# Kernel tuning notes

Hardware: AMD Instinct MI355X
Metric: run time of the kernel (lower is better)

The kernel has to match this reference:

```python
import jax, jax.numpy as jnp
import numpy as np

B, L, D, H = 2, 2048, 1024, 16
HD = D // H
ROPE_BASE = 10000.0


def _chain_info(lengths):
    """lengths: [B, L] int, chain lengths packed at the front, zeros after.
    Returns per-position within-chain positions (RoPE resets per chain),
    chain ids, and a validity mask."""
    def one(row):
        csum = jnp.cumsum(row)                      # [L]
        total = csum[-1]
        p = jnp.arange(L)
        cid = jnp.searchsorted(csum, p, side='right')  # chain id per position
        prev = jnp.where(cid > 0, csum[jnp.clip(cid - 1, 0, L - 1)], 0)
        valid = p < total
        pos = jnp.where(valid, p - prev, 0).astype(jnp.float32)
        return pos, cid, valid
    return jax.vmap(one)(lengths)


def _rope_tables(pos):
    # pos: [B, L] float -> cos/sin [B, L, 1, HD]
    inv_freq = 1.0 / (ROPE_BASE ** (jnp.arange(0, HD, 2, dtype=jnp.float32) / HD))
    freqs = pos[..., None] * inv_freq               # [B, L, HD/2]
    emb = jnp.concatenate([freqs, freqs], axis=-1)  # [B, L, HD]
    return jnp.cos(emb)[:, :, None, :], jnp.sin(emb)[:, :, None, :]


def _apply_rope(x, cos, sin):
    d = x.shape[-1]
    x1, x2 = x[..., : d // 2], x[..., d // 2:]
    return x * cos + jnp.concatenate([-x2, x1], axis=-1) * sin


def _branch(x, Wqkv, bqkv, cos, sin, allowed):
    # x: [B, L, D]; allowed: [B, L, L] bool attention mask for this branch
    qkv = x @ Wqkv.T + bqkv                          # [B, L, 3D]
    qkv = qkv.reshape(B, L, 3, H, HD)
    q, k, v = qkv[:, :, 0], qkv[:, :, 1], qkv[:, :, 2]
    q = q * (HD ** -0.5)
    q = _apply_rope(q, cos, sin)
    k = _apply_rope(k, cos, sin)
    scores = jnp.einsum('bthd,bshd->bhts', q, k)     # [B, H, L, L]
    scores = jnp.where(allowed[:, None], scores, -jnp.inf)
    probs = jax.nn.softmax(scores, axis=-1)
    probs = jnp.where(jnp.isnan(probs), 0.0, probs)  # fully-masked rows -> 0
    out = jnp.einsum('bhts,bshd->bthd', probs, v)    # [B, L, H, HD]
    return out.reshape(B, L, D)


def setup_inputs() -> dict:
    key = jax.random.key(0)
    ks = jax.random.split(key, 7)
    s = 0.02
    lens = np.zeros((B, L), np.int64)
    lens[0, :8] = [300, 250, 200, 400, 350, 248, 150, 100]   # sum 1998
    lens[1, :6] = [512, 400, 300, 360, 276, 200]             # sum 2048
    return {
        'hidden_states': jax.random.normal(ks[0], (B, L, D), jnp.float32),
        'attention_mask_in_length': jnp.asarray(lens),
        'Wqkv_intra': jax.random.normal(ks[1], (3 * D, D), jnp.float32) * s,
        'bqkv_intra': jnp.zeros((3 * D,), jnp.float32),
        'Wqkv_inter': jax.random.normal(ks[2], (3 * D, D), jnp.float32) * s,
        'bqkv_inter': jnp.zeros((3 * D,), jnp.float32),
        'Wout': jax.random.normal(ks[3], (D, D), jnp.float32) * s,
        'bout': jnp.zeros((D,), jnp.float32),
    }


def reference(hidden_states, attention_mask_in_length, Wqkv_intra, bqkv_intra,
              Wqkv_inter, bqkv_inter, Wout, bout):
    pos, cid, valid = _chain_info(attention_mask_in_length)
    cos, sin = _rope_tables(pos)
    same_chain = cid[:, :, None] == cid[:, None, :]          # [B, L, L]
    key_valid = valid[:, None, :]                            # [B, 1, L]
    allowed_intra = same_chain & key_valid
    allowed_inter = (~same_chain) & key_valid
    out_intra = _branch(hidden_states, Wqkv_intra, bqkv_intra, cos, sin, allowed_intra)
    out_inter = _branch(hidden_states, Wqkv_inter, bqkv_inter, cos, sin, allowed_inter)
    return (out_intra + out_inter) @ Wout.T + bout
```

## Files before the change

kernel.cpp:

```cpp
#include <hip/hip_runtime.h>
#include <hip/hip_bf16.h>
#include <stdint.h>

#define B 2
#define L 2048
#define D 1024
#define H 16
#define HD 64
#define NT (L / 64)
#define INVALID_CID 0x40000000

typedef __hip_bfloat16 bf16;
typedef __attribute__((ext_vector_type(8))) short short8;
typedef __attribute__((ext_vector_type(4))) float floatx4;

static __device__ __forceinline__ short f2bf(float f) {
    bf16 h = __float2bfloat16(f);
    return *reinterpret_cast<short*>(&h);
}

static __device__ __forceinline__ void async_copy16(const void* g, void* l) {
    __builtin_amdgcn_global_load_lds((__attribute__((address_space(1))) void*)g,
                                     (__attribute__((address_space(3))) void*)l,
                                     16, 0, 0);
}

__global__ void chain_kernel(const int* __restrict__ lens,
                             float* __restrict__ pos, int* __restrict__ cid,
                             int4* __restrict__ tinfo)
{
    __shared__ int csum[L];
    __shared__ int cids[L];
    __shared__ int part[256];
    int b = blockIdx.x;
    int t = threadIdx.x;

    int loc[8];
    int s = 0;
    #pragma unroll
    for (int j = 0; j < 8; ++j) { s += lens[b * L + t * 8 + j]; loc[j] = s; }
    part[t] = s;
    __syncthreads();
    if (t == 0) {
        int acc = 0;
        for (int i = 0; i < 256; ++i) { int v = part[i]; part[i] = acc; acc += v; }
    }
    __syncthreads();
    int base = part[t];
    #pragma unroll
    for (int j = 0; j < 8; ++j) csum[t * 8 + j] = base + loc[j];
    __syncthreads();

    int total = csum[L - 1];
    for (int p = t; p < L; p += 256) {
        int cv;
        if (p < total) {
            int lo = 0, hi = L;
            while (lo < hi) {
                int mid = (lo + hi) >> 1;
                if (csum[mid] <= p) lo = mid + 1; else hi = mid;
            }
            int prev = (lo > 0) ? csum[lo - 1] : 0;
            pos[b * L + p] = (float)(p - prev);
            cv = lo;
        } else {
            pos[b * L + p] = 0.f;
            cv = INVALID_CID;
        }
        cids[p] = cv;
        cid[b * L + p] = cv;
    }
    __syncthreads();
    if (t < NT) {
        int mn = 0x7fffffff, mx = -1, any = 0, all = 1;
        for (int j = 0; j < 64; ++j) {
            int cv = cids[t * 64 + j];
            if (cv != INVALID_CID) { any = 1; mn = min(mn, cv); mx = max(mx, cv); }
            else all = 0;
        }
        tinfo[b * NT + t] = make_int4(mn, mx, any | (all << 1), 0);
    }
}

__global__ void cast_f32_bf16(const float* __restrict__ in, bf16* __restrict__ out, int n)
{
    int i = (blockIdx.x * 256 + threadIdx.x) * 4;
    if (i + 3 < n) {
        float4 v = *(const float4*)(in + i);
        out[i + 0] = __float2bfloat16(v.x);
        out[i + 1] = __float2bfloat16(v.y);
        out[i + 2] = __float2bfloat16(v.z);
        out[i + 3] = __float2bfloat16(v.w);
    } else {
        for (; i < n; ++i) out[i] = __float2bfloat16(in[i]);
    }
}

__global__ __launch_bounds__(256, 4) void gemm128(
    const bf16* __restrict__ A, const bf16* __restrict__ Bw,
    const float* __restrict__ bias, void* __restrict__ Cout,
    int M, int N, int K, int c_bf16)
{
    __shared__ short As[128 * 32];
    __shared__ short Bs[128 * 32];

    int tid = threadIdx.x;
    int wave = tid >> 6, lane = tid & 63;
    int i15 = lane & 15, q8 = lane >> 4;
    int wm = wave & 1, wn = wave >> 1;
    int m0 = blockIdx.y * 128, n0 = blockIdx.x * 128;

    floatx4 acc[4][4];
    #pragma unroll
    for (int mt = 0; mt < 4; ++mt)
        #pragma unroll
        for (int nt = 0; nt < 4; ++nt) acc[mt][nt] = (floatx4){0.f, 0.f, 0.f, 0.f};

    const short* gA = (const short*)A  + (size_t)(m0 + wave * 32 + (lane >> 2)) * K + (lane & 3) * 8;
    const short* gB = (const short*)Bw + (size_t)(n0 + wave * 32 + (lane >> 2)) * K + (lane & 3) * 8;
    short* lA = As + wave * 1024;
    short* lB = Bs + wave * 1024;

    for (int kt = 0; kt < K; kt += 32) {
        __syncthreads();
        async_copy16(gA + kt,          lA);
        async_copy16(gA + 16 * K + kt, lA + 512);
        async_copy16(gB + kt,          lB);
        async_copy16(gB + 16 * K + kt, lB + 512);
        __syncthreads();

        short8 af[4], bfr[4];
        #pragma unroll
        for (int mt = 0; mt < 4; ++mt)
            af[mt] = *(const short8*)&As[(wm * 64 + mt * 16 + i15) * 32 + q8 * 8];
        #pragma unroll
        for (int nt = 0; nt < 4; ++nt)
            bfr[nt] = *(const short8*)&Bs[(wn * 64 + nt * 16 + i15) * 32 + q8 * 8];
        #pragma unroll
        for (int mt = 0; mt < 4; ++mt)
            #pragma unroll
            for (int nt = 0; nt < 4; ++nt)
                acc[mt][nt] = __builtin_amdgcn_mfma_f32_16x16x32_bf16(af[mt], bfr[nt], acc[mt][nt], 0, 0, 0);
    }

    #pragma unroll
    for (int nt = 0; nt < 4; ++nt) {
        int n = n0 + wn * 64 + nt * 16 + i15;
        float bv = bias[n];
        #pragma unroll
        for (int mt = 0; mt < 4; ++mt) {
            #pragma unroll
            for (int rg = 0; rg < 4; ++rg) {
                int m = m0 + wm * 64 + mt * 16 + q8 * 4 + rg;
                float v = acc[mt][nt][rg] + bv;
                if (c_bf16) ((bf16*)Cout)[(size_t)m * N + n] = __float2bfloat16(v);
                else        ((float*)Cout)[(size_t)m * N + n] = v;
            }
        }
    }
}

__global__ __launch_bounds__(256) void rope_scatter2(
    const bf16* __restrict__ qkv, const float* __restrict__ pos,
    bf16* __restrict__ Qo, bf16* __restrict__ Ko, bf16* __restrict__ Vtg)
{
    __shared__ float Vsh[64][65];
    int tid = threadIdx.x;
    int bid = blockIdx.x;
    int lt = bid & (NT - 1);
    int h  = (bid >> 5) & (H - 1);
    int b  = bid >> 9;
    int l0 = lt * 64;

    const float QSCALE = 0.18033688011111772f;
    int hd = tid & 63, lq = tid >> 6;
    float sgn = (hd < 32) ? -1.f : 1.f;
    float invf = exp2f(-(float)(hd & 31) * (13.287712379549449f / 32.f));

    #pragma unroll
    for (int rr = 0; rr < 16; ++rr) {
        int l = l0 + lq * 16 + rr;
        size_t row = (size_t)(b * L + l) * (3 * D);
        int col  = h * HD + hd;
        int col2 = h * HD + (hd ^ 32);

        float xq  = __bfloat162float(qkv[row + col]);
        float xq2 = __bfloat162float(qkv[row + col2]);
        float xk  = __bfloat162float(qkv[row + D + col]);
        float xk2 = __bfloat162float(qkv[row + D + col2]);
        float xv  = __bfloat162float(qkv[row + 2 * D + col]);

        float p = pos[b * L + l];
        float ang = p * invf;
        float cc = cosf(ang), ss = sinf(ang);

        float qo = QSCALE * (xq * cc + sgn * xq2 * ss);
        float ko = xk * cc + sgn * xk2 * ss;

        size_t o = ((size_t)(b * H + h) * L + l) * HD + hd;
        Qo[o] = __float2bfloat16(qo);
        Ko[o] = __float2bfloat16(ko);
        Vsh[l - l0][hd] = xv;
    }
    __syncthreads();
    int lcol = tid & 63, dq = tid >> 6;
    #pragma unroll
    for (int rr = 0; rr < 16; ++rr) {
        int dd = dq * 16 + rr;
        Vtg[((size_t)(b * H + h) * HD + dd) * L + l0 + lcol] = __float2bfloat16(Vsh[lcol][dd]);
    }
}

__global__ __launch_bounds__(256, 4) void attn2(
    const bf16* __restrict__ Q, const bf16* __restrict__ Kg, const bf16* __restrict__ Vtg,
    const int* __restrict__ cid, const int4* __restrict__ tinfo,
    float* __restrict__ OutF, bf16* __restrict__ OutB, const float* __restrict__ Prev,
    int branch)
{
    __shared__ short Ks[64][72];
    __shared__ short Vs[64][72];
    __shared__ short Ps[64][72];
    __shared__ int cls_s[NT];
    __shared__ int list_s[NT];
    __shared__ int nlist_s;

    int tid = threadIdx.x;
    int wave = tid >> 6, lane = tid & 63;
    int i15 = lane & 15, q8 = lane >> 4;
    int bid = blockIdx.x;
    int qt = bid & (NT - 1);
    int h  = (bid >> 5) & (H - 1);
    int b  = bid >> 9;
    int q0 = qt * 64;
    const size_t bh  = (size_t)(b * H + h) * L;
    const size_t bhd = (size_t)(b * H + h) * HD;

    short8 afq[2];
    {
        const short* qp = (const short*)Q + (bh + q0 + wave * 16 + i15) * HD + q8 * 8;
        afq[0] = *(const short8*)(qp);
        afq[1] = *(const short8*)(qp + 32);
    }
    int cqv[4];
    #pragma unroll
    for (int rg = 0; rg < 4; ++rg) cqv[rg] = cid[b * L + q0 + wave * 16 + q8 * 4 + rg];

    int4 qinf = tinfo[b * NT + qt];
    int qall = (qinf.z >> 1) & 1;

    if (tid < NT) {
        int4 ki = tinfo[b * NT + tid];
        int kany = ki.z & 1, kall = (ki.z >> 1) & 1;
        bool disjoint = (ki.x > qinf.y) || (ki.y < qinf.x);
        bool mono = qall && kall && (qinf.x == qinf.y) && (ki.x == ki.y) && (qinf.x == ki.x);
        int cls;
        if (branch == 0) {
            if (!kany || disjoint) cls = 0;
            else if (mono) cls = 2;
            else cls = 1;
        } else {
            if (!kany || mono) cls = 0;
            else if (kall && disjoint) cls = 2;
            else cls = 1;
        }
        cls_s[tid] = cls;
    }
    __syncthreads();
    if (tid == 0) {
        int n = 0;
        for (int t = 0; t < NT; ++t) {
            int c = cls_s[t];
            if (c) list_s[n++] = (t * 64) | ((c == 2) << 16);
        }
        nlist_s = n;
    }
    __syncthreads();
    int n = nlist_s;

    int r = tid >> 2, ccol = (tid & 3) * 16;
    const short* Kbase = (const short*)Kg  + (bh + r) * HD + ccol;
    const short* Vbase = (const short*)Vtg + (bhd + r) * L + ccol;

    int4 pk0, pk1, pv0, pv1;
    int cur = 0;
    if (n > 0) {
        cur = list_s[0];
        int kt = cur & 0xffff;
        pk0 = *(const int4*)(Kbase + (size_t)kt * HD);
        pk1 = *(const int4*)(Kbase + (size_t)kt * HD + 8);
        pv0 = *(const int4*)(Vbase + kt);
        pv1 = *(const int4*)(Vbase + kt + 8);
    }

    floatx4 accO[4];
    #pragma unroll
    for (int t = 0; t < 4; ++t) accO[t] = (floatx4){0.f, 0.f, 0.f, 0.f};
    float lsum[4] = {0.f, 0.f, 0.f, 0.f};

    for (int i = 0; i < n; ++i) {
        int kt = cur & 0xffff, full = cur >> 16;

        __syncthreads();
        *(int4*)&Ks[r][ccol]     = pk0;
        *(int4*)&Ks[r][ccol + 8] = pk1;
        *(int4*)&Vs[r][ccol]     = pv0;
        *(int4*)&Vs[r][ccol + 8] = pv1;
        __syncthreads();

        if (i + 1 < n) {
            cur = list_s[i + 1];
            int nk = cur & 0xffff;
            pk0 = *(const int4*)(Kbase + (size_t)nk * HD);
            pk1 = *(const int4*)(Kbase + (size_t)nk * HD + 8);
            pv0 = *(const int4*)(Vbase + nk);
            pv1 = *(const int4*)(Vbase + nk + 8);
        }

        floatx4 accS[4];
        #pragma unroll
        for (int t = 0; t < 4; ++t) accS[t] = (floatx4){0.f, 0.f, 0.f, 0.f};
        #pragma unroll
        for (int s = 0; s < 2; ++s) {
            #pragma unroll
            for (int t = 0; t < 4; ++t) {
                short8 bfr = *(const short8*)&Ks[t * 16 + i15][s * 32 + q8 * 8];
                accS[t] = __builtin_amdgcn_mfma_f32_16x16x32_bf16(afq[s], bfr, accS[t], 0, 0, 0);
            }
        }

        if (!full) {
            #pragma unroll
            for (int t = 0; t < 4; ++t) {
                int ck = cid[b * L + kt + t * 16 + i15];
                bool kv = (ck != INVALID_CID);
                #pragma unroll
                for (int rg = 0; rg < 4; ++rg) {
                    bool match = (cqv[rg] == ck);
                    bool ok = kv && (branch ? !match : match);
                    accS[t][rg] = ok ? accS[t][rg] : -1e30f;
                }
            }
        }

        #pragma unroll
        for (int t = 0; t < 4; ++t) {
            #pragma unroll
            for (int rg = 0; rg < 4; ++rg) {
                float p = __builtin_amdgcn_exp2f(accS[t][rg]);
                lsum[rg] += p;
                Ps[wave * 16 + q8 * 4 + rg][t * 16 + i15] = f2bf(p);
            }
        }

        #pragma unroll
        for (int s = 0; s < 2; ++s) {
            short8 af2 = *(const short8*)&Ps[wave * 16 + i15][s * 32 + q8 * 8];
            #pragma unroll
            for (int t = 0; t < 4; ++t) {
                short8 bfr = *(const short8*)&Vs[t * 16 + i15][s * 32 + q8 * 8];
                accO[t] = __builtin_amdgcn_mfma_f32_16x16x32_bf16(af2, bfr, accO[t], 0, 0, 0);
            }
        }
    }

    #pragma unroll
    for (int rg = 0; rg < 4; ++rg) {
        #pragma unroll
        for (int d = 1; d < 16; d <<= 1)
            lsum[rg] += __shfl_xor(lsum[rg], d, 64);
    }
    float inv[4];
    #pragma unroll
    for (int rg = 0; rg < 4; ++rg) inv[rg] = (lsum[rg] > 0.f) ? 1.f / lsum[rg] : 0.f;

    #pragma unroll
    for (int t = 0; t < 4; ++t) {
        #pragma unroll
        for (int rg = 0; rg < 4; ++rg) {
            size_t idx = (size_t)(b * L + q0 + wave * 16 + q8 * 4 + rg) * D + h * HD + t * 16 + i15;
            float o = accO[t][rg] * inv[rg];
            if (branch == 0) OutF[idx] = o;
            else             OutB[idx] = __float2bfloat16(o + Prev[idx]);
        }
    }
}

extern "C" void kernel_launch(void* const* d_in, const int* in_sizes, int n_in,
                              void* d_out, int out_size, void* d_ws, size_t ws_size,
                              hipStream_t stream)
{
    const float* x    = (const float*)d_in[0];
    const int*   mlen = (const int*)  d_in[1];
    const float* Wi   = (const float*)d_in[2];
    const float* bi   = (const float*)d_in[3];
    const float* We   = (const float*)d_in[4];
    const float* be   = (const float*)d_in[5];
    const float* Wo   = (const float*)d_in[6];
    const float* bo   = (const float*)d_in[7];

    char* ws = (char*)d_ws;
    size_t off = 0;
    auto alloc = [&](size_t bytes) {
        void* p = ws + off;
        off += (bytes + 255) & ~(size_t)255;
        return p;
    };
    bf16*  x_b   = (bf16*) alloc((size_t)B * L * D * 2);
    bf16*  Wi_b  = (bf16*) alloc((size_t)3 * D * D * 2);
    bf16*  We_b  = (bf16*) alloc((size_t)3 * D * D * 2);
    bf16*  Wo_b  = (bf16*) alloc((size_t)D * D * 2);
    bf16*  qkv_b = (bf16*) alloc((size_t)B * L * 3 * D * 2);
    bf16*  q_b   = (bf16*) alloc((size_t)B * H * L * HD * 2);
    bf16*  k_b   = (bf16*) alloc((size_t)B * H * L * HD * 2);
    bf16*  vt_b  = (bf16*) alloc((size_t)B * H * HD * L * 2);
    float* att_i = (float*)alloc((size_t)B * L * D * 4);
    bf16*  sum_b = (bf16*) alloc((size_t)B * L * D * 2);
    float* pos   = (float*)alloc((size_t)B * L * 4);
    int*   cid   = (int*)  alloc((size_t)B * L * 4);
    int4*  tinfo = (int4*) alloc((size_t)B * NT * 16);
    (void)ws_size; (void)n_in; (void)in_sizes; (void)out_size;

    chain_kernel<<<B, 256, 0, stream>>>(mlen, pos, cid, tinfo);

    int nx = B * L * D;
    int nw = 3 * D * D;
    cast_f32_bf16<<<(nx / 4 + 255) / 256, 256, 0, stream>>>(x, x_b, nx);
    cast_f32_bf16<<<(nw / 4 + 255) / 256, 256, 0, stream>>>(Wi, Wi_b, nw);
    cast_f32_bf16<<<(nw / 4 + 255) / 256, 256, 0, stream>>>(We, We_b, nw);
    cast_f32_bf16<<<(D * D / 4 + 255) / 256, 256, 0, stream>>>(Wo, Wo_b, D * D);

    dim3 gq(3 * D / 128, B * L / 128);
    gemm128<<<gq, 256, 0, stream>>>(x_b, Wi_b, bi, qkv_b, B * L, 3 * D, D, 1);
    rope_scatter2<<<B * H * NT, 256, 0, stream>>>(qkv_b, pos, q_b, k_b, vt_b);
    attn2<<<B * H * NT, 256, 0, stream>>>(q_b, k_b, vt_b, cid, tinfo, att_i, sum_b, att_i, 0);

    gemm128<<<gq, 256, 0, stream>>>(x_b, We_b, be, qkv_b, B * L, 3 * D, D, 1);
    rope_scatter2<<<B * H * NT, 256, 0, stream>>>(qkv_b, pos, q_b, k_b, vt_b);
    attn2<<<B * H * NT, 256, 0, stream>>>(q_b, k_b, vt_b, cid, tinfo, att_i, sum_b, att_i, 1);

    dim3 go(D / 128, B * L / 128);
    gemm128<<<go, 256, 0, stream>>>(sum_b, Wo_b, bo, d_out, B * L, D, D, 0);
}
```

Baseline: 348.9 us.

## Restructure attention with 32x32 MFMA, register-resident K/V, and split-K waves

Rewrites the attention kernel so each wave computes a 32x32 score tile with 32x32x16 MFMAs (S^T = K·Q^T). K and V fragments are loaded straight from global memory into registers, and P stays in registers instead of going through LDS. Waves split the key dimension in two, and the halves are reduced through LDS at the end. Block index is remapped so neighboring blocks spread across heads for cache locality. This removes the per-tile LDS staging and barriers. The cost is direct global loads without software prefetch, plus an extra LDS reduction and the risk of exposed load latency.

After: 433.6 us. 1.24x slower.

```diff
diff --git a/kernel.cpp b/kernel.cpp
--- a/kernel.cpp
+++ b/kernel.cpp
@@ -12,7 +12,9 @@
 
 typedef __hip_bfloat16 bf16;
 typedef __attribute__((ext_vector_type(8))) short short8;
+typedef __attribute__((ext_vector_type(4))) short short4v;
 typedef __attribute__((ext_vector_type(4))) float floatx4;
+typedef __attribute__((ext_vector_type(16))) float floatx16;
 
 static __device__ __forceinline__ short f2bf(float f) {
     bf16 h = __float2bfloat16(f);
@@ -211,39 +213,39 @@
     }
 }
 
-__global__ __launch_bounds__(256, 4) void attn2(
+__global__ __launch_bounds__(256, 4) void attn3(
     const bf16* __restrict__ Q, const bf16* __restrict__ Kg, const bf16* __restrict__ Vtg,
     const int* __restrict__ cid, const int4* __restrict__ tinfo,
     float* __restrict__ OutF, bf16* __restrict__ OutB, const float* __restrict__ Prev,
     int branch)
 {
-    __shared__ short Ks[64][72];
-    __shared__ short Vs[64][72];
-    __shared__ short Ps[64][72];
+    __shared__ float Of[2][64][65];
+    __shared__ float ls[2][64];
     __shared__ int cls_s[NT];
     __shared__ int list_s[NT];
     __shared__ int nlist_s;
 
     int tid = threadIdx.x;
     int wave = tid >> 6, lane = tid & 63;
-    int i15 = lane & 15, q8 = lane >> 4;
+    int l31 = lane & 31, l5 = lane >> 5;
+    int kw = wave & 1, qw = wave >> 1;
+
     int bid = blockIdx.x;
-    int qt = bid & (NT - 1);
-    int h  = (bid >> 5) & (H - 1);
-    int b  = bid >> 9;
+    int bh_idx = (bid & 7) * 4 + ((bid >> 3) >> 5);
+    int qt = (bid >> 3) & 31;
+    int h = bh_idx & (H - 1);
+    int b = bh_idx >> 4;
     int q0 = qt * 64;
     const size_t bh  = (size_t)(b * H + h) * L;
     const size_t bhd = (size_t)(b * H + h) * HD;
 
-    short8 afq[2];
+    short8 qf[4];
     {
-        const short* qp = (const short*)Q + (bh + q0 + wave * 16 + i15) * HD + q8 * 8;
-        afq[0] = *(const short8*)(qp);
-        afq[1] = *(const short8*)(qp + 32);
-    }
-    int cqv[4];
-    #pragma unroll
-    for (int rg = 0; rg < 4; ++rg) cqv[rg] = cid[b * L + q0 + wave * 16 + q8 * 4 + rg];
+        const short* qp = (const short*)Q + (bh + q0 + qw * 32 + l31) * HD + l5 * 8;
+        #pragma unroll
+        for (int c = 0; c < 4; ++c) qf[c] = *(const short8*)(qp + c * 16);
+    }
+    int cq = cid[b * L + q0 + qw * 32 + l31];
 
     int4 qinf = tinfo[b * NT + qt];
     int qall = (qinf.z >> 1) & 1;
@@ -277,110 +279,100 @@
     __syncthreads();
     int n = nlist_s;
 
-    int r = tid >> 2, ccol = (tid & 3) * 16;
-    const short* Kbase = (const short*)Kg  + (bh + r) * HD + ccol;
-    const short* Vbase = (const short*)Vtg + (bhd + r) * L + ccol;
-
-    int4 pk0, pk1, pv0, pv1;
-    int cur = 0;
-    if (n > 0) {
-        cur = list_s[0];
-        int kt = cur & 0xffff;
-        pk0 = *(const int4*)(Kbase + (size_t)kt * HD);
-        pk1 = *(const int4*)(Kbase + (size_t)kt * HD + 8);
-        pv0 = *(const int4*)(Vbase + kt);
-        pv1 = *(const int4*)(Vbase + kt + 8);
-    }
-
-    floatx4 accO[4];
-    #pragma unroll
-    for (int t = 0; t < 4; ++t) accO[t] = (floatx4){0.f, 0.f, 0.f, 0.f};
-    float lsum[4] = {0.f, 0.f, 0.f, 0.f};
-
-    for (int i = 0; i < n; ++i) {
+    int kidx = (l31 & 0x13) | ((l31 & 4) << 1) | ((l31 & 8) >> 1);
+    const short* kbase = (const short*)Kg  + (bh + kw * 32 + kidx) * HD + l5 * 8;
+    const short* vbase = (const short*)Vtg + (bhd + l31) * L + kw * 32 + l5 * 8;
+
+    floatx16 accO[2];
+    #pragma unroll
+    for (int r = 0; r < 16; ++r) { accO[0][r] = 0.f; accO[1][r] = 0.f; }
+    float lsum = 0.f;
+
+    for (int it = 0; it < n; ++it) {
+        int cur = list_s[it];
         int kt = cur & 0xffff, full = cur >> 16;
 
-        __syncthreads();
-        *(int4*)&Ks[r][ccol]     = pk0;
-        *(int4*)&Ks[r][ccol + 8] = pk1;
-        *(int4*)&Vs[r][ccol]     = pv0;
-        *(int4*)&Vs[r][ccol + 8] = pv1;
-        __syncthreads();
-
-        if (i + 1 < n) {
-            cur = list_s[i + 1];
-            int nk = cur & 0xffff;
-            pk0 = *(const int4*)(Kbase + (size_t)nk * HD);
-            pk1 = *(const int4*)(Kbase + (size_t)nk * HD + 8);
-            pv0 = *(const int4*)(Vbase + nk);
-            pv1 = *(const int4*)(Vbase + nk + 8);
-        }
-
-        floatx4 accS[4];
-        #pragma unroll
-        for (int t = 0; t < 4; ++t) accS[t] = (floatx4){0.f, 0.f, 0.f, 0.f};
-        #pragma unroll
-        for (int s = 0; s < 2; ++s) {
+        short8 kf[4], vf[2][2];
+        {
+            const short* kp = kbase + (size_t)kt * HD;
             #pragma unroll
-            for (int t = 0; t < 4; ++t) {
-                short8 bfr = *(const short8*)&Ks[t * 16 + i15][s * 32 + q8 * 8];
-                accS[t] = __builtin_amdgcn_mfma_f32_16x16x32_bf16(afq[s], bfr, accS[t], 0, 0, 0);
-            }
-        }
+            for (int c = 0; c < 4; ++c) kf[c] = *(const short8*)(kp + c * 16);
+            #pragma unroll
+            for (int dt = 0; dt < 2; ++dt)
+                #pragma unroll
+                for (int c = 0; c < 2; ++c)
+                    vf[dt][c] = *(const short8*)(vbase + (size_t)dt * 32 * L + kt + c * 16);
+        }
+
+        floatx16 accS;
+        #pragma unroll
+        for (int r = 0; r < 16; ++r) accS[r] = 0.f;
+        #pragma unroll
+        for (int c = 0; c < 4; ++c)
+            accS = __builtin_amdgcn_mfma_f32_32x32x16_bf16(kf[c], qf[c], accS, 0, 0, 0);
 
         if (!full) {
             #pragma unroll
-            for (int t = 0; t < 4; ++t) {
-                int ck = cid[b * L + kt + t * 16 + i15];
-                bool kv = (ck != INVALID_CID);
+            for (int g = 0; g < 4; ++g) {
+                int koff = kt + kw * 32 + 4 * (g & 1) + 8 * l5 + 16 * (g >> 1);
+                int4 kc = *(const int4*)&cid[b * L + koff];
+                int ckk[4] = {kc.x, kc.y, kc.z, kc.w};
                 #pragma unroll
-                for (int rg = 0; rg < 4; ++rg) {
-                    bool match = (cqv[rg] == ck);
+                for (int j = 0; j < 4; ++j) {
+                    bool kv = (ckk[j] != INVALID_CID);
+                    bool match = (cq == ckk[j]);
                     bool ok = kv && (branch ? !match : match);
-                    accS[t][rg] = ok ? accS[t][rg] : -1e30f;
+                    int r = g * 4 + j;
+                    accS[r] = ok ? accS[r] : -1e30f;
                 }
             }
         }
 
-        #pragma unroll
-        for (int t = 0; t < 4; ++t) {
-            #pragma unroll
-            for (int rg = 0; rg < 4; ++rg) {
-                float p = __builtin_amdgcn_exp2f(accS[t][rg]);
-                lsum[rg] += p;
-                Ps[wave * 16 + q8 * 4 + rg][t * 16 + i15] = f2bf(p);
-            }
-        }
-
-        #pragma unroll
-        for (int s = 0; s < 2; ++s) {
-            short8 af2 = *(const short8*)&Ps[wave * 16 + i15][s * 32 + q8 * 8];
-            #pragma unroll
-            for (int t = 0; t < 4; ++t) {
-                short8 bfr = *(const short8*)&Vs[t * 16 + i15][s * 32 + q8 * 8];
-                accO[t] = __builtin_amdgcn_mfma_f32_16x16x32_bf16(af2, bfr, accO[t], 0, 0, 0);
-            }
-        }
-    }
-
-    #pragma unroll
-    for (int rg = 0; rg < 4; ++rg) {
-        #pragma unroll
-        for (int d = 1; d < 16; d <<= 1)
-            lsum[rg] += __shfl_xor(lsum[rg], d, 64);
-    }
-    float inv[4];
-    #pragma unroll
-    for (int rg = 0; rg < 4; ++rg) inv[rg] = (lsum[rg] > 0.f) ? 1.f / lsum[rg] : 0.f;
-
-    #pragma unroll
-    for (int t = 0; t < 4; ++t) {
-        #pragma unroll
-        for (int rg = 0; rg < 4; ++rg) {
-            size_t idx = (size_t)(b * L + q0 + wave * 16 + q8 * 4 + rg) * D + h * HD + t * 16 + i15;
-            float o = accO[t][rg] * inv[rg];
-            if (branch == 0) OutF[idx] = o;
-            else             OutB[idx] = __float2bfloat16(o + Prev[idx]);
+        short p16[16];
+        #pragma unroll
+        for (int r = 0; r < 16; ++r) {
+            float p = __builtin_amdgcn_exp2f(accS[r]);
+            lsum += p;
+            p16[r] = f2bf(p);
+        }
+        short8 pf0 = {p16[0], p16[1], p16[2],  p16[3],  p16[4],  p16[5],  p16[6],  p16[7]};
+        short8 pf1 = {p16[8], p16[9], p16[10], p16[11], p16[12], p16[13], p16[14], p16[15]};
+
+        #pragma unroll
+        for (int dt = 0; dt < 2; ++dt) {
+            accO[dt] = __builtin_amdgcn_mfma_f32_32x32x16_bf16(pf0, vf[dt][0], accO[dt], 0, 0, 0);
+            accO[dt] = __builtin_amdgcn_mfma_f32_32x32x16_bf16(pf1, vf[dt][1], accO[dt], 0, 0, 0);
+        }
+    }
+
+    lsum += __shfl_xor(lsum, 32, 64);
+    if (l5 == 0) ls[kw][qw * 32 + l31] = lsum;
+    #pragma unroll
+    for (int dt = 0; dt < 2; ++dt)
+        #pragma unroll
+        for (int r = 0; r < 16; ++r) {
+            int q = (r & 3) + 8 * (r >> 2) + 4 * l5;
+            Of[kw][qw * 32 + q][dt * 32 + l31] = accO[dt][r];
+        }
+    __syncthreads();
+
+    int q = tid & 63, dg = tid >> 6;
+    float lt2 = ls[0][q] + ls[1][q];
+    float invl = (lt2 > 0.f) ? 1.f / lt2 : 0.f;
+    #pragma unroll
+    for (int v = 0; v < 4; ++v) {
+        int d = dg * 16 + v * 4;
+        float4 o0 = *(const float4*)&Of[0][q][d];
+        float4 o1 = *(const float4*)&Of[1][q][d];
+        size_t idx = (size_t)(b * L + q0 + q) * D + h * HD + d;
+        float ox = (o0.x + o1.x) * invl, oy = (o0.y + o1.y) * invl;
+        float oz = (o0.z + o1.z) * invl, ow = (o0.w + o1.w) * invl;
+        if (branch == 0) {
+            *(float4*)&OutF[idx] = make_float4(ox, oy, oz, ow);
+        } else {
+            float4 pv = *(const float4*)&Prev[idx];
+            short4v st = {f2bf(ox + pv.x), f2bf(oy + pv.y), f2bf(oz + pv.z), f2bf(ow + pv.w)};
+            *(short4v*)&OutB[idx] = st;
         }
     }
 }
@@ -432,11 +424,11 @@
     dim3 gq(3 * D / 128, B * L / 128);
     gemm128<<<gq, 256, 0, stream>>>(x_b, Wi_b, bi, qkv_b, B * L, 3 * D, D, 1);
     rope_scatter2<<<B * H * NT, 256, 0, stream>>>(qkv_b, pos, q_b, k_b, vt_b);
-    attn2<<<B * H * NT, 256, 0, stream>>>(q_b, k_b, vt_b, cid, tinfo, att_i, sum_b, att_i, 0);
+    attn3<<<B * H * NT, 256, 0, stream>>>(q_b, k_b, vt_b, cid, tinfo, att_i, sum_b, att_i, 0);
 
     gemm128<<<gq, 256, 0, stream>>>(x_b, We_b, be, qkv_b, B * L, 3 * D, D, 1);
     rope_scatter2<<<B * H * NT, 256, 0, stream>>>(qkv_b, pos, q_b, k_b, vt_b);
-    attn2<<<B * H * NT, 256, 0, stream>>>(q_b, k_b, vt_b, cid, tinfo, att_i, sum_b, att_i, 1);
+    attn3<<<B * H * NT, 256, 0, stream>>>(q_b, k_b, vt_b, cid, tinfo, att_i, sum_b, att_i, 1);
 
     dim3 go(D / 128, B * L / 128);
     gemm128<<<go, 256, 0, stream>>>(sum_b, Wo_b, bo, d_out, B * L, D, D, 0);
```
